# Kernel optimization log

Measured on AMD Instinct MI355X. Metric: run time of the kernel, lower is better.

The kernel has to match this reference:

```python
import jax, jax.numpy as jnp
import numpy as np

N, K = 16384, 1024  # samples, classes == feature dim


def setup_inputs() -> dict:
    key = jax.random.key(0)
    k1, k2 = jax.random.split(key)
    x = jax.random.normal(k1, (N, K), dtype=jnp.float32)
    # mu initialized like 100*one_hot plus noise so normalization is non-trivial
    mu = 100.0 * jnp.eye(K, dtype=jnp.float32) + jax.random.normal(k2, (K, K), dtype=jnp.float32)
    std = jnp.full((K,), 1.0 / K, dtype=jnp.float32)  # diag(eye(K)) * 1/K
    return {"x": x, "mu": mu, "std": std}


def reference(x, mu, std):
    # mu normalized per-row (as in forward)
    mu_n = mu / jnp.linalg.norm(mu, axis=-1, keepdims=True)  # [M, K]
    inv_std = 1.0 / std  # [K]
    # Mahalanobis-style squared distance with diagonal covariance, via GEMM expansion:
    xx = (x * x) @ inv_std                                  # [N]
    mm = jnp.sum(mu_n * mu_n * inv_std[None, :], axis=-1)   # [M]
    cross = x @ (mu_n * inv_std[None, :]).T                 # [N, M]
    logits = -0.5 * (xx[:, None] + mm[None, :] - 2.0 * cross)
    return logits
```

## Files before the change

kernel.cpp:

```cpp
#include <hip/hip_runtime.h>

typedef __attribute__((ext_vector_type(8))) int   i32x8;
typedef __attribute__((ext_vector_type(4))) float f32x4;
typedef unsigned int uint32;

constexpr int N = 16384;
constexpr int K = 1024;
constexpr int M = 1024;

#define WAITVM(n) asm volatile("s_waitcnt vmcnt(" #n ")" ::: "memory")
#define FENCE() asm volatile("" ::: "memory")
#define BAR()                          \
    do {                               \
        FENCE();                       \
        __builtin_amdgcn_s_barrier();  \
        FENCE();                       \
    } while (0)

__device__ inline void gload_lds16(const unsigned char* g, unsigned char* l) {
    __builtin_amdgcn_global_load_lds(
        (const __attribute__((address_space(1))) unsigned int*)g,
        (__attribute__((address_space(3))) unsigned int*)l,
        16, 0, 0);
}

__device__ inline uint32 pack4_fp8(float a, float b, float c, float d) {
    int v = __builtin_amdgcn_cvt_pk_fp8_f32(a, b, 0, false);
    v = __builtin_amdgcn_cvt_pk_fp8_f32(c, d, v, true);
    return (uint32)v;
}

__global__ void prep_mu(const float* __restrict__ mu, const float* __restrict__ stdv,
                        uint32* __restrict__ Wb8, float* __restrict__ mmh) {
    int m = blockIdx.x;
    int t = threadIdx.x;
    float4 v = ((const float4*)(mu + (size_t)m * K))[t];
    float4 s = ((const float4*)stdv)[t];
    float ix = 1.0f / s.x, iy = 1.0f / s.y, iz = 1.0f / s.z, iw = 1.0f / s.w;
    float sum2  = v.x * v.x + v.y * v.y + v.z * v.z + v.w * v.w;
    float sum2w = v.x * v.x * ix + v.y * v.y * iy + v.z * v.z * iz + v.w * v.w * iw;
    for (int off = 32; off > 0; off >>= 1) {
        sum2  += __shfl_down(sum2, off, 64);
        sum2w += __shfl_down(sum2w, off, 64);
    }
    __shared__ float r2[4], r2w[4];
    __shared__ float s_scale;
    int lane = t & 63, w = t >> 6;
    if (lane == 0) { r2[w] = sum2; r2w[w] = sum2w; }
    __syncthreads();
    if (t == 0) {
        float tot2  = r2[0] + r2[1] + r2[2] + r2[3];
        float tot2w = r2w[0] + r2w[1] + r2w[2] + r2w[3];
        mmh[m] = -0.5f * tot2w / tot2;
        s_scale = rsqrtf(tot2) * 0.25f;
    }
    __syncthreads();
    float sc = s_scale;
    Wb8[m * (K / 4) + t] = pack4_fp8(v.x * ix * sc, v.y * iy * sc,
                                     v.z * iz * sc, v.w * iw * sc);
}

__global__ __launch_bounds__(256) void prep_x(const float* __restrict__ x,
                                              const float* __restrict__ stdv,
                                              uint32* __restrict__ xb8,
                                              float* __restrict__ xxh) {
    int row = blockIdx.x * 4 + (threadIdx.x >> 6);
    int lane = threadIdx.x & 63;
    const float4* src = (const float4*)(x + (size_t)row * K);
    const float4* sp  = (const float4*)stdv;
    uint32* dst = xb8 + (size_t)row * (K / 4);
    float ssum = 0.f;
#pragma unroll
    for (int i = 0; i < 4; ++i) {
        int idx = lane + 64 * i;
        float4 v = src[idx];
        float4 s = sp[idx];
        ssum += v.x * v.x / s.x + v.y * v.y / s.y + v.z * v.z / s.z + v.w * v.w / s.w;
        dst[idx] = pack4_fp8(v.x, v.y, v.z, v.w);
    }
#pragma unroll
    for (int off = 32; off > 0; off >>= 1) ssum += __shfl_down(ssum, off, 64);
    if (lane == 0) xxh[row] = -0.5f * ssum;
}

#define BKB 128
#define TILEB (128 * BKB)

__global__ __launch_bounds__(256, 2) void gemm_ep(
    const unsigned char* __restrict__ A8, const unsigned char* __restrict__ B8,
    const float* __restrict__ xxh, const float* __restrict__ mmh,
    float* __restrict__ C) {
    __shared__ unsigned char Als[2 * TILEB];
    __shared__ unsigned char Bls[2 * TILEB];

    int t = threadIdx.x;
    int lane = t & 63;
    int wave = t >> 6;
    int wr = wave >> 1;
    int wc = wave & 1;
    int r  = lane & 15;
    int lk = lane >> 4;

    int bid = blockIdx.x;
    int swz = (bid & 7) * 128 + (bid >> 3);
    int tn = swz >> 3;
    int tm = swz & 7;

    const unsigned char* Abase = A8 + (size_t)tn * 128 * K;
    const unsigned char* Bbase = B8 + (size_t)tm * 128 * K;

    f32x4 acc[4][4] = {};

#define STAGE(kt_, buf_)                                                       \
    {                                                                          \
        const unsigned char* Ag_ = Abase + (size_t)(kt_)*BKB;                  \
        const unsigned char* Bg_ = Bbase + (size_t)(kt_)*BKB;                  \
        unsigned char* Al_ = Als + (buf_)*TILEB;                               \
        unsigned char* Bl_ = Bls + (buf_)*TILEB;                               \
        _Pragma("unroll")                                                      \
        for (int i_ = 0; i_ < 4; ++i_) {                                       \
            int c_ = i_ * 256 + t;                                             \
            int row_ = c_ >> 3;                                                \
            int gs_ = (c_ & 7) ^ (row_ & 7);                                   \
            gload_lds16(Ag_ + (size_t)row_ * K + gs_ * 16,                     \
                        Al_ + (i_ * 256 + wave * 64) * 16);                    \
        }                                                                      \
        _Pragma("unroll")                                                      \
        for (int i_ = 0; i_ < 4; ++i_) {                                       \
            int c_ = i_ * 256 + t;                                             \
            int row_ = c_ >> 3;                                                \
            int gs_ = (c_ & 7) ^ (row_ & 7);                                   \
            gload_lds16(Bg_ + (size_t)row_ * K + gs_ * 16,                     \
                        Bl_ + (i_ * 256 + wave * 64) * 16);                    \
        }                                                                      \
    }

    STAGE(0, 0);
    WAITVM(0);
    BAR();

    const int NT = K / BKB;
    for (int kt = 0; kt < NT; ++kt) {
        int cur = kt & 1;
        if (kt + 1 < NT) STAGE(kt + 1, cur ^ 1);

        const unsigned char* As = Als + cur * TILEB;
        const unsigned char* Bs = Bls + cur * TILEB;

        i32x8 af[4], bf[4];
#pragma unroll
        for (int mi = 0; mi < 4; ++mi) {
            int row = wr * 64 + mi * 16 + r;
            uint4 q0 = *(const uint4*)&As[row * BKB + (((lk << 1) | 0) ^ (r & 7)) * 16];
            uint4 q1 = *(const uint4*)&As[row * BKB + (((lk << 1) | 1) ^ (r & 7)) * 16];
            af[mi][0] = q0.x; af[mi][1] = q0.y; af[mi][2] = q0.z; af[mi][3] = q0.w;
            af[mi][4] = q1.x; af[mi][5] = q1.y; af[mi][6] = q1.z; af[mi][7] = q1.w;
        }
#pragma unroll
        for (int ni = 0; ni < 4; ++ni) {
            int row = wc * 64 + ni * 16 + r;
            uint4 q0 = *(const uint4*)&Bs[row * BKB + (((lk << 1) | 0) ^ (r & 7)) * 16];
            uint4 q1 = *(const uint4*)&Bs[row * BKB + (((lk << 1) | 1) ^ (r & 7)) * 16];
            bf[ni][0] = q0.x; bf[ni][1] = q0.y; bf[ni][2] = q0.z; bf[ni][3] = q0.w;
            bf[ni][4] = q1.x; bf[ni][5] = q1.y; bf[ni][6] = q1.z; bf[ni][7] = q1.w;
        }

        __builtin_amdgcn_s_setprio(1);
#pragma unroll
        for (int mi = 0; mi < 4; ++mi)
#pragma unroll
            for (int ni = 0; ni < 4; ++ni)
                acc[mi][ni] = __builtin_amdgcn_mfma_scale_f32_16x16x128_f8f6f4(
                    af[mi], bf[ni], acc[mi][ni],
                    0, 0,
                    0, 0x7f7f7f7f,
                    0, 0x7f7f7f7f);
        __builtin_amdgcn_s_setprio(0);

        if (kt + 1 < NT) WAITVM(0);
        BAR();
    }

    int rowb = tn * 128 + wr * 64;
    int colb = tm * 128 + wc * 64;
#pragma unroll
    for (int mi = 0; mi < 4; ++mi) {
        float xh[4];
#pragma unroll
        for (int j = 0; j < 4; ++j) xh[j] = xxh[rowb + mi * 16 + lk * 4 + j];
#pragma unroll
        for (int ni = 0; ni < 4; ++ni) {
            int col = colb + ni * 16 + r;
            float mh = mmh[col];
#pragma unroll
            for (int j = 0; j < 4; ++j) {
                int row = rowb + mi * 16 + lk * 4 + j;
                C[(size_t)row * M + col] = acc[mi][ni][j] * 4.0f + xh[j] + mh;
            }
        }
    }
#undef STAGE
}

extern "C" void kernel_launch(void* const* d_in, const int* in_sizes, int n_in,
                              void* d_out, int out_size, void* d_ws, size_t ws_size,
                              hipStream_t stream) {
    const float* x    = (const float*)d_in[0];
    const float* mu   = (const float*)d_in[1];
    const float* stdv = (const float*)d_in[2];
    float* out = (float*)d_out;

    char* ws = (char*)d_ws;
    unsigned char* xb8 = (unsigned char*)ws;
    unsigned char* Wb8 = (unsigned char*)(ws + (size_t)N * K);
    float* xxh = (float*)(ws + (size_t)N * K + (size_t)M * K);
    float* mmh = (float*)((char*)xxh + (size_t)N * sizeof(float));

    prep_mu<<<M, 256, 0, stream>>>(mu, stdv, (uint32*)Wb8, mmh);
    prep_x<<<N / 4, 256, 0, stream>>>(x, stdv, (uint32*)xb8, xxh);
    gemm_ep<<<(N / 128) * (M / 128), 256, 0, stream>>>(xb8, Wb8, xxh, mmh, out);
}
```

Measured before the change: 49.80 us.

## Load B operand fragments directly from global memory, stage only A in LDS

The GEMM no longer stages B tiles through shared memory. Each wave reads its B fragments straight from global memory (relying on L2, since B is small and heavily reused), while A stays double-buffered in LDS. This halves LDS use, which permits raising launch bounds to three blocks per SM. In exchange, the B global loads sit on the critical path right before the MFMAs with no prefetch, and the wait on vmcnt(0) now also waits for them, which may expose memory latency.

```diff
diff --git a/kernel.cpp b/kernel.cpp
--- a/kernel.cpp
+++ b/kernel.cpp
@@ -84,14 +84,13 @@
 }
 
 #define BKB 128
-#define TILEB (128 * BKB)
-
-__global__ __launch_bounds__(256, 2) void gemm_ep(
+#define ATILE (128 * BKB)
+
+__global__ __launch_bounds__(256, 3) void gemm_ep(
     const unsigned char* __restrict__ A8, const unsigned char* __restrict__ B8,
     const float* __restrict__ xxh, const float* __restrict__ mmh,
     float* __restrict__ C) {
-    __shared__ unsigned char Als[2 * TILEB];
-    __shared__ unsigned char Bls[2 * TILEB];
+    __shared__ unsigned char Als[2 * ATILE];
 
     int t = threadIdx.x;
     int lane = t & 63;
@@ -111,58 +110,50 @@
 
     f32x4 acc[4][4] = {};
 
-#define STAGE(kt_, buf_)                                                       \
+#define STAGE_A(kt_, buf_)                                                     \
     {                                                                          \
-        const unsigned char* Ag_ = Abase + (size_t)(kt_)*BKB;                  \
-        const unsigned char* Bg_ = Bbase + (size_t)(kt_)*BKB;                  \
-        unsigned char* Al_ = Als + (buf_)*TILEB;                               \
-        unsigned char* Bl_ = Bls + (buf_)*TILEB;                               \
+        const unsigned char* g_ = Abase + (size_t)(kt_) * BKB;                 \
+        unsigned char* l_ = Als + (buf_) * ATILE;                              \
         _Pragma("unroll")                                                      \
         for (int i_ = 0; i_ < 4; ++i_) {                                       \
             int c_ = i_ * 256 + t;                                             \
             int row_ = c_ >> 3;                                                \
-            int gs_ = (c_ & 7) ^ (row_ & 7);                                   \
-            gload_lds16(Ag_ + (size_t)row_ * K + gs_ * 16,                     \
-                        Al_ + (i_ * 256 + wave * 64) * 16);                    \
+            int slot_ = (c_ & 7) ^ (row_ & 7);                                 \
+            gload_lds16(g_ + (size_t)row_ * K + slot_ * 16,                    \
+                        l_ + (i_ * 256 + (wave << 6)) * 16);                   \
         }                                                                      \
-        _Pragma("unroll")                                                      \
-        for (int i_ = 0; i_ < 4; ++i_) {                                       \
-            int c_ = i_ * 256 + t;                                             \
-            int row_ = c_ >> 3;                                                \
-            int gs_ = (c_ & 7) ^ (row_ & 7);                                   \
-            gload_lds16(Bg_ + (size_t)row_ * K + gs_ * 16,                     \
-                        Bl_ + (i_ * 256 + wave * 64) * 16);                    \
-        }                                                                      \
-    }
-
-    STAGE(0, 0);
+    }
+
+    STAGE_A(0, 0);
     WAITVM(0);
     BAR();
 
     const int NT = K / BKB;
     for (int kt = 0; kt < NT; ++kt) {
         int cur = kt & 1;
-        if (kt + 1 < NT) STAGE(kt + 1, cur ^ 1);
-
-        const unsigned char* As = Als + cur * TILEB;
-        const unsigned char* Bs = Bls + cur * TILEB;
-
-        i32x8 af[4], bf[4];
+        const unsigned char* As = Als + cur * ATILE;
+
+        if (kt + 1 < NT) STAGE_A(kt + 1, cur ^ 1);
+
+        i32x8 bf[4];
+#pragma unroll
+        for (int ni = 0; ni < 4; ++ni) {
+            const unsigned char* brow =
+                Bbase + (size_t)(wc * 64 + ni * 16 + r) * K + (size_t)kt * BKB;
+            uint4 q0 = *(const uint4*)(brow + lk * 32);
+            uint4 q1 = *(const uint4*)(brow + lk * 32 + 16);
+            bf[ni][0] = q0.x; bf[ni][1] = q0.y; bf[ni][2] = q0.z; bf[ni][3] = q0.w;
+            bf[ni][4] = q1.x; bf[ni][5] = q1.y; bf[ni][6] = q1.z; bf[ni][7] = q1.w;
+        }
+
+        i32x8 af[4];
 #pragma unroll
         for (int mi = 0; mi < 4; ++mi) {
             int row = wr * 64 + mi * 16 + r;
-            uint4 q0 = *(const uint4*)&As[row * BKB + (((lk << 1) | 0) ^ (r & 7)) * 16];
-            uint4 q1 = *(const uint4*)&As[row * BKB + (((lk << 1) | 1) ^ (r & 7)) * 16];
+            uint4 q0 = *(const uint4*)&As[(row << 7) + ((((lk << 1) | 0) ^ (r & 7)) << 4)];
+            uint4 q1 = *(const uint4*)&As[(row << 7) + ((((lk << 1) | 1) ^ (r & 7)) << 4)];
             af[mi][0] = q0.x; af[mi][1] = q0.y; af[mi][2] = q0.z; af[mi][3] = q0.w;
             af[mi][4] = q1.x; af[mi][5] = q1.y; af[mi][6] = q1.z; af[mi][7] = q1.w;
-        }
-#pragma unroll
-        for (int ni = 0; ni < 4; ++ni) {
-            int row = wc * 64 + ni * 16 + r;
-            uint4 q0 = *(const uint4*)&Bs[row * BKB + (((lk << 1) | 0) ^ (r & 7)) * 16];
-            uint4 q1 = *(const uint4*)&Bs[row * BKB + (((lk << 1) | 1) ^ (r & 7)) * 16];
-            bf[ni][0] = q0.x; bf[ni][1] = q0.y; bf[ni][2] = q0.z; bf[ni][3] = q0.w;
-            bf[ni][4] = q1.x; bf[ni][5] = q1.y; bf[ni][6] = q1.z; bf[ni][7] = q1.w;
         }
 
         __builtin_amdgcn_s_setprio(1);
@@ -199,7 +190,7 @@
             }
         }
     }
-#undef STAGE
+#undef STAGE_A
 }
 
 extern "C" void kernel_launch(void* const* d_in, const int* in_sizes, int n_in,
```

Result: slower. 66.63 us (+33.8%).
